# Kernel optimization log

Hardware: AMD Instinct MI355X
Metric: run time of the kernel (lower is better)

The kernel has to match this reference:

```python
import jax, jax.numpy as jnp
import numpy as np

B, N, D, H = 2, 2048, 1024, 16
HD = D // H

def setup_inputs() -> dict:
    key = jax.random.key(0)
    ks = jax.random.split(key, 5)
    s_in = 1.0 / np.sqrt(D)
    x = jax.random.normal(ks[0], (B, N, D), dtype=jnp.float32)
    W_qkv = jax.random.uniform(ks[1], (3 * D, D), minval=-s_in, maxval=s_in, dtype=jnp.float32)
    b_qkv = jax.random.uniform(ks[2], (3 * D,), minval=-s_in, maxval=s_in, dtype=jnp.float32)
    W_out = jax.random.uniform(ks[3], (D, D), minval=-s_in, maxval=s_in, dtype=jnp.float32)
    b_out = jax.random.uniform(ks[4], (D,), minval=-s_in, maxval=s_in, dtype=jnp.float32)
    return {"x": x, "W_qkv": W_qkv, "b_qkv": b_qkv, "W_out": W_out, "b_out": b_out}

def reference(x, W_qkv, b_qkv, W_out, b_out):
    scale = HD ** (-0.5)
    qkv = x @ W_qkv.T + b_qkv                       # [B,N,3D]
    q, k, v = jnp.split(qkv, 3, axis=-1)
    # [B,N,D] -> [B,H,N,HD]
    def heads(t):
        return t.reshape(B, N, H, HD).transpose(0, 2, 1, 3)
    q, k, v = heads(q), heads(k), heads(v)
    attn = jnp.einsum('bhqd,bhkd->bhqk', q, k) * scale   # [B,H,N,N]
    causal = jnp.tril(jnp.ones((N, N), dtype=bool))
    attn = jnp.where(causal, attn, -jnp.inf)
    attn = jax.nn.softmax(attn, axis=-1)
    out = jnp.einsum('bhqk,bhkd->bhqd', attn, v)         # [B,H,N,HD]
    out = out.transpose(0, 2, 1, 3).reshape(B, N, D)
    return out @ W_out.T + b_out
```

## Files before the change

kernel.cpp:

```cpp
#include <hip/hip_runtime.h>
#include <hip/hip_bf16.h>

#define Bdim 2
#define Nseq 2048
#define Dmod 1024
#define Hn   16
#define HDim 64

#define XN  (Bdim * Nseq * Dmod)
#define WQN (3 * Dmod * Dmod)
#define WON (Dmod * Dmod)

typedef __attribute__((ext_vector_type(8))) __bf16 bf16x8;
typedef __attribute__((ext_vector_type(4))) __bf16 bf16x4;
typedef __attribute__((ext_vector_type(4))) float  floatx4;

__device__ __forceinline__ floatx4 mfma16(bf16x8 a, bf16x8 b, floatx4 c) {
    return __builtin_amdgcn_mfma_f32_16x16x32_bf16(a, b, c, 0, 0, 0);
}

__device__ __forceinline__ float exp2v(float x) {
    return __builtin_amdgcn_exp2f(x);
}

__device__ __forceinline__ void async_copy16(__bf16* l, const __bf16* g) {
    __builtin_amdgcn_global_load_lds(
        (const __attribute__((address_space(1))) void*)g,
        (__attribute__((address_space(3))) void*)l,
        16, 0, 0);
}

__global__ __launch_bounds__(256) void convert_kernel(
    const float* __restrict__ x, const float* __restrict__ wq,
    const float* __restrict__ wo,
    __bf16* __restrict__ xb, __bf16* __restrict__ wqb, __bf16* __restrict__ wob)
{
    int i = (blockIdx.x * 256 + threadIdx.x) * 8;
    const float* src;
    __bf16* dst;
    int off;
    if (i < XN)            { src = x;  dst = xb;  off = i; }
    else if (i < XN + WQN) { src = wq; dst = wqb; off = i - XN; }
    else                   { src = wo; dst = wob; off = i - XN - WQN; }
    float4 v0 = *(const float4*)(src + off);
    float4 v1 = *(const float4*)(src + off + 4);
    bf16x8 o;
    o[0] = (__bf16)v0.x; o[1] = (__bf16)v0.y; o[2] = (__bf16)v0.z; o[3] = (__bf16)v0.w;
    o[4] = (__bf16)v1.x; o[5] = (__bf16)v1.y; o[6] = (__bf16)v1.z; o[7] = (__bf16)v1.w;
    *(bf16x8*)(dst + off) = o;
}

__global__ __launch_bounds__(256) void qkv_kernel(
    const __bf16* __restrict__ x, const __bf16* __restrict__ Wq,
    const float* __restrict__ bq,
    __bf16* __restrict__ qb, __bf16* __restrict__ kb, __bf16* __restrict__ vt)
{
    __shared__ __align__(16) __bf16 ldsA[128 * 32];
    __shared__ __align__(16) __bf16 ldsB[128 * 32];

    const int tid  = threadIdx.x;
    const int lane = tid & 63, l16 = lane & 15, quad = lane >> 4;
    const int wiw  = tid >> 6;
    const int wm   = wiw & 1, wn = wiw >> 1;

    const int bm = blockIdx.x & 31;
    const int bn = blockIdx.x >> 5;
    const int m0 = bm * 128, n0 = bn * 128;

    const int srow = tid >> 2;
    const int scol = (tid & 3) * 8;

    floatx4 z = {0.f, 0.f, 0.f, 0.f};
    floatx4 acc[4][4];
    #pragma unroll
    for (int mt = 0; mt < 4; ++mt)
        #pragma unroll
        for (int nt = 0; nt < 4; ++nt) acc[mt][nt] = z;

    const __bf16* ga = x  + (size_t)m0 * Dmod;
    const __bf16* gb = Wq + (size_t)n0 * Dmod;

    for (int k0 = 0; k0 < Dmod; k0 += 32) {
        async_copy16(&ldsA[srow * 32 + scol],        ga + (size_t)srow * Dmod + k0 + scol);
        async_copy16(&ldsA[(64 + srow) * 32 + scol], ga + (size_t)(64 + srow) * Dmod + k0 + scol);
        async_copy16(&ldsB[srow * 32 + scol],        gb + (size_t)srow * Dmod + k0 + scol);
        async_copy16(&ldsB[(64 + srow) * 32 + scol], gb + (size_t)(64 + srow) * Dmod + k0 + scol);
        __syncthreads();

        bf16x8 af[4], bfr[4];
        #pragma unroll
        for (int mt = 0; mt < 4; ++mt)
            af[mt] = *(const bf16x8*)&ldsA[(wm * 64 + mt * 16 + l16) * 32 + quad * 8];
        #pragma unroll
        for (int nt = 0; nt < 4; ++nt)
            bfr[nt] = *(const bf16x8*)&ldsB[(wn * 64 + nt * 16 + l16) * 32 + quad * 8];
        #pragma unroll
        for (int mt = 0; mt < 4; ++mt)
            #pragma unroll
            for (int nt = 0; nt < 4; ++nt)
                acc[mt][nt] = mfma16(af[mt], bfr[nt], acc[mt][nt]);
        __syncthreads();
    }

    const int nb    = n0 + wn * 64;
    const int which = nb >> 10;
    const int h     = (nb & 1023) >> 6;
    const int mw    = m0 + wm * 64;
    const int bi    = mw >> 11;
    const int pos0  = mw & (Nseq - 1);

    const float qscale = 0.18033688f;

    #pragma unroll
    for (int nt = 0; nt < 4; ++nt) {
        float bias = bq[nb + nt * 16 + l16];
        int hd = nt * 16 + l16;
        #pragma unroll
        for (int mt = 0; mt < 4; ++mt)
            #pragma unroll
            for (int i = 0; i < 4; ++i) {
                int pos = pos0 + mt * 16 + quad * 4 + i;
                float r = acc[mt][nt][i] + bias;
                if (which == 0)
                    qb[((bi * Hn + h) * Nseq + pos) * HDim + hd] = (__bf16)(r * qscale);
                else if (which == 1)
                    kb[((bi * Hn + h) * Nseq + pos) * HDim + hd] = (__bf16)r;
                else
                    vt[((bi * Hn + h) * HDim + hd) * Nseq + pos] = (__bf16)r;
            }
    }
}

__global__ __launch_bounds__(256, 4) void attn_kernel(
    const __bf16* __restrict__ qbuf, const __bf16* __restrict__ kbuf,
    const __bf16* __restrict__ vtbuf, __bf16* __restrict__ aout)
{
    __shared__ __align__(16) __bf16 ldsK[64 * 64];
    __shared__ __align__(16) __bf16 ldsV[64 * 64];
    __shared__ __align__(16) __bf16 ldsP[4][16 * 72];

    const int tid  = threadIdx.x;
    const int wiw  = tid >> 6;
    const int lane = tid & 63, l16 = lane & 15, quad = lane >> 4;
    const int b    = blockIdx.x;
    const int bh   = b & 31;
    const int g  = b >> 5;
    const int gk = g & 7, r4 = g >> 3;
    int qblk;
    if      (r4 == 0) qblk = 31 - gk;
    else if (r4 == 1) qblk = gk;
    else if (r4 == 2) qblk = 23 - gk;
    else              qblk = 8 + gk;

    const int q0 = qblk * 64 + wiw * 16;

    const __bf16* qs = qbuf  + bh * Nseq * HDim;
    const __bf16* ks = kbuf  + bh * Nseq * HDim;
    const __bf16* vs = vtbuf + bh * HDim * Nseq;

    const int sr  = tid >> 3;
    const int sb  = tid & 7;
    const int swr = (sb ^ (sr & 7)) * 8;
    const int wk0 = sr * 64 + swr;
    const int wk1 = (sr + 32) * 64 + swr;

    bf16x8 qf0 = *(const bf16x8*)(qs + (q0 + l16) * HDim + quad * 8);
    bf16x8 qf1 = *(const bf16x8*)(qs + (q0 + l16) * HDim + 32 + quad * 8);

    floatx4 z = {0.f, 0.f, 0.f, 0.f};
    floatx4 o[4];
    #pragma unroll
    for (int s = 0; s < 4; ++s) o[s] = z;
    floatx4 lacc = z;
    float m_i = -1e30f;

    bf16x8 ones;
    #pragma unroll
    for (int j = 0; j < 8; ++j) ones[j] = (__bf16)1.0f;

    const int   nkt = qblk + 1;
    __bf16* myp = ldsP[wiw];
    const int swz = l16 & 7;

    float4 rk0 = *(const float4*)(ks + (size_t)sr * HDim + sb * 8);
    float4 rk1 = *(const float4*)(ks + (size_t)(sr + 32) * HDim + sb * 8);
    float4 rv0 = *(const float4*)(vs + (size_t)sr * Nseq + sb * 8);
    float4 rv1 = *(const float4*)(vs + (size_t)(sr + 32) * Nseq + sb * 8);

    for (int kt = 0; kt < nkt; ++kt) {
        float4 nk0 = {}, nk1 = {}, nv0 = {}, nv1 = {};
        if (kt + 1 < nkt) {
            const int k0n = (kt + 1) * 64;
            nk0 = *(const float4*)(ks + (size_t)(k0n + sr) * HDim + sb * 8);
            nk1 = *(const float4*)(ks + (size_t)(k0n + sr + 32) * HDim + sb * 8);
            nv0 = *(const float4*)(vs + (size_t)sr * Nseq + k0n + sb * 8);
            nv1 = *(const float4*)(vs + (size_t)(sr + 32) * Nseq + k0n + sb * 8);
        }

        *(float4*)&ldsK[wk0] = rk0;
        *(float4*)&ldsK[wk1] = rk1;
        *(float4*)&ldsV[wk0] = rv0;
        *(float4*)&ldsV[wk1] = rv1;
        __syncthreads();

        const bool last = (kt == nkt - 1);

        floatx4 st[4];
        __builtin_amdgcn_s_setprio(1);
        #pragma unroll
        for (int t = 0; t < 4; ++t) {
            const __bf16* kr = &ldsK[(t * 16 + l16) * 64];
            bf16x8 kf0 = *(const bf16x8*)(kr + ((quad ^ swz) * 8));
            bf16x8 kf1 = *(const bf16x8*)(kr + (((quad + 4) ^ swz) * 8));
            st[t] = mfma16(kf0, qf0, z);
            st[t] = mfma16(kf1, qf1, st[t]);
        }
        __builtin_amdgcn_s_setprio(0);

        float a[16];
        #pragma unroll
        for (int t = 0; t < 4; ++t)
            #pragma unroll
            for (int i = 0; i < 4; ++i) {
                float v = st[t][i];
                if (last) {
                    int kidx = t * 16 + quad * 4 + i;
                    v = (kidx <= wiw * 16 + l16) ? v : -1e30f;
                }
                a[t * 4 + i] = v;
            }

        float m0 = fmaxf(fmaxf(a[0],  a[1]),  a[2]);
        float m1 = fmaxf(fmaxf(a[3],  a[4]),  a[5]);
        float m2 = fmaxf(fmaxf(a[6],  a[7]),  a[8]);
        float m3 = fmaxf(fmaxf(a[9],  a[10]), a[11]);
        float m4 = fmaxf(fmaxf(a[12], a[13]), a[14]);
        float mx = fmaxf(fmaxf(fmaxf(m0, m1), m2),
                         fmaxf(fmaxf(m3, m4), a[15]));
        mx = fmaxf(mx, __shfl_xor(mx, 16));
        mx = fmaxf(mx, __shfl_xor(mx, 32));

        if (__any(mx > m_i + 8.0f)) {
            float mn    = fmaxf(m_i, mx);
            float alpha = exp2v(m_i - mn);
            #pragma unroll
            for (int s = 0; s < 4; ++s)
                #pragma unroll
                for (int i = 0; i < 4; ++i) o[s][i] *= alpha;
            #pragma unroll
            for (int i = 0; i < 4; ++i) lacc[i] *= alpha;
            m_i = mn;
        }

        float p[16];
        #pragma unroll
        for (int j = 0; j < 16; ++j) p[j] = exp2v(a[j] - m_i);

        #pragma unroll
        for (int t = 0; t < 4; ++t) {
            bf16x4 pk;
            pk.x = (__bf16)p[t * 4 + 0]; pk.y = (__bf16)p[t * 4 + 1];
            pk.z = (__bf16)p[t * 4 + 2]; pk.w = (__bf16)p[t * 4 + 3];
            *(bf16x4*)(myp + l16 * 72 + t * 16 + quad * 4) = pk;
        }
        asm volatile("s_waitcnt lgkmcnt(0)" ::: "memory");
        bf16x8 pf0 = *(const bf16x8*)(myp + l16 * 72 + quad * 8);
        bf16x8 pf1 = *(const bf16x8*)(myp + l16 * 72 + 32 + quad * 8);

        __builtin_amdgcn_s_setprio(1);
        lacc = mfma16(ones, pf0, lacc);
        lacc = mfma16(ones, pf1, lacc);

        #pragma unroll
        for (int s = 0; s < 4; ++s) {
            const __bf16* vr = &ldsV[(s * 16 + l16) * 64];
            bf16x8 vf0 = *(const bf16x8*)(vr + ((quad ^ swz) * 8));
            bf16x8 vf1 = *(const bf16x8*)(vr + (((quad + 4) ^ swz) * 8));
            o[s] = mfma16(vf0, pf0, o[s]);
            o[s] = mfma16(vf1, pf1, o[s]);
        }
        __builtin_amdgcn_s_setprio(0);
        __syncthreads();

        rk0 = nk0; rk1 = nk1; rv0 = nv0; rv1 = nv1;
    }

    const float inv = 1.0f / lacc[0];
    const int bi = bh >> 4, h = bh & 15;
    #pragma unroll
    for (int s = 0; s < 4; ++s) {
        bf16x4 ov;
        ov.x = (__bf16)(o[s][0] * inv); ov.y = (__bf16)(o[s][1] * inv);
        ov.z = (__bf16)(o[s][2] * inv); ov.w = (__bf16)(o[s][3] * inv);
        *(bf16x4*)(aout + ((size_t)(bi * Nseq + q0 + l16)) * Dmod
                   + h * 64 + s * 16 + quad * 4) = ov;
    }
}

__global__ __launch_bounds__(256) void proj_kernel(
    const __bf16* __restrict__ ao, const __bf16* __restrict__ Wo,
    const float* __restrict__ bo, float* __restrict__ out)
{
    __shared__ __align__(16) __bf16 ldsA[64 * 32];
    __shared__ __align__(16) __bf16 ldsB[128 * 32];

    const int tid  = threadIdx.x;
    const int lane = tid & 63, l16 = lane & 15, quad = lane >> 4;
    const int wiw  = tid >> 6;
    const int wm   = wiw & 1, wn = wiw >> 1;

    const int bm = blockIdx.x & 63;
    const int bn = blockIdx.x >> 6;
    const int m0 = bm * 64, n0 = bn * 128;

    const int srow = tid >> 2;
    const int scol = (tid & 3) * 8;

    floatx4 z = {0.f, 0.f, 0.f, 0.f};
    floatx4 acc[2][4];
    #pragma unroll
    for (int mt = 0; mt < 2; ++mt)
        #pragma unroll
        for (int nt = 0; nt < 4; ++nt) acc[mt][nt] = z;

    const __bf16* ga = ao + (size_t)m0 * Dmod;
    const __bf16* gb = Wo + (size_t)n0 * Dmod;

    for (int k0 = 0; k0 < Dmod; k0 += 32) {
        async_copy16(&ldsA[srow * 32 + scol],        ga + (size_t)srow * Dmod + k0 + scol);
        async_copy16(&ldsB[srow * 32 + scol],        gb + (size_t)srow * Dmod + k0 + scol);
        async_copy16(&ldsB[(64 + srow) * 32 + scol], gb + (size_t)(64 + srow) * Dmod + k0 + scol);
        __syncthreads();

        bf16x8 af[2], bfr[4];
        #pragma unroll
        for (int mt = 0; mt < 2; ++mt)
            af[mt] = *(const bf16x8*)&ldsA[(wm * 32 + mt * 16 + l16) * 32 + quad * 8];
        #pragma unroll
        for (int nt = 0; nt < 4; ++nt)
            bfr[nt] = *(const bf16x8*)&ldsB[(wn * 64 + nt * 16 + l16) * 32 + quad * 8];
        #pragma unroll
        for (int mt = 0; mt < 2; ++mt)
            #pragma unroll
            for (int nt = 0; nt < 4; ++nt)
                acc[mt][nt] = mfma16(af[mt], bfr[nt], acc[mt][nt]);
        __syncthreads();
    }

    const int nb = n0 + wn * 64;
    const int mw = m0 + wm * 32;
    #pragma unroll
    for (int nt = 0; nt < 4; ++nt) {
        float bias = bo[nb + nt * 16 + l16];
        #pragma unroll
        for (int mt = 0; mt < 2; ++mt)
            #pragma unroll
            for (int i = 0; i < 4; ++i) {
                int m = mw + mt * 16 + quad * 4 + i;
                out[(size_t)m * Dmod + nb + nt * 16 + l16] = acc[mt][nt][i] + bias;
            }
    }
}

extern "C" void kernel_launch(void* const* d_in, const int* in_sizes, int n_in,
                              void* d_out, int out_size, void* d_ws, size_t ws_size,
                              hipStream_t stream) {
    const float* x  = (const float*)d_in[0];
    const float* Wq = (const float*)d_in[1];
    const float* bq = (const float*)d_in[2];
    const float* Wo = (const float*)d_in[3];
    const float* bo = (const float*)d_in[4];
    float* out = (float*)d_out;

    __bf16* ws  = (__bf16*)d_ws;
    __bf16* xb  = ws;
    __bf16* wqb = ws + (size_t)XN;
    __bf16* wob = wqb + (size_t)WQN;
    __bf16* qb  = wob + (size_t)WON;
    const size_t SZ = (size_t)Bdim * Hn * Nseq * HDim;
    __bf16* kb  = qb + SZ;
    __bf16* vt  = kb + SZ;
    __bf16* ao  = vt + SZ;

    convert_kernel<<<dim3(4096), dim3(256), 0, stream>>>(x, Wq, Wo, xb, wqb, wob);
    qkv_kernel<<<dim3(768), dim3(256), 0, stream>>>(xb, wqb, bq, qb, kb, vt);
    attn_kernel<<<dim3(1024), dim3(256), 0, stream>>>(qb, kb, vt, ao);
    proj_kernel<<<dim3(512), dim3(256), 0, stream>>>(ao, wob, bo, out);
}
```

Before: 174.5 us.

## Double K-tile depth with XOR-swizzled LDS and XCD-aware block mapping in GEMMs

The QKV and output-projection GEMMs now stage 64-wide K slices per iteration instead of 32, which halves the number of barrier pairs per K sweep. Each LDS row gets an XOR swizzle on its 16-byte chunks so the fragment reads avoid bank conflicts. Block indices are also remapped: in the QKV GEMM each XCD is given a contiguous group of N-tiles, and the projection GEMM walks N fastest, both to improve L2 reuse of the weights. LDS use per block doubles, which may lower occupancy.

```diff
diff --git a/kernel.cpp b/kernel.cpp
--- a/kernel.cpp
+++ b/kernel.cpp
@@ -55,20 +55,24 @@
     const float* __restrict__ bq,
     __bf16* __restrict__ qb, __bf16* __restrict__ kb, __bf16* __restrict__ vt)
 {
-    __shared__ __align__(16) __bf16 ldsA[128 * 32];
-    __shared__ __align__(16) __bf16 ldsB[128 * 32];
+    __shared__ __align__(16) __bf16 ldsA[128 * 64];
+    __shared__ __align__(16) __bf16 ldsB[128 * 64];
 
     const int tid  = threadIdx.x;
     const int lane = tid & 63, l16 = lane & 15, quad = lane >> 4;
     const int wiw  = tid >> 6;
     const int wm   = wiw & 1, wn = wiw >> 1;
-
-    const int bm = blockIdx.x & 31;
-    const int bn = blockIdx.x >> 5;
+    const int swq  = l16 & 7;
+
+    const int xcd = blockIdx.x & 7;
+    const int loc = blockIdx.x >> 3;
+    const int bn  = xcd * 3 + loc % 3;
+    const int bm  = loc / 3;
     const int m0 = bm * 128, n0 = bn * 128;
 
-    const int srow = tid >> 2;
-    const int scol = (tid & 3) * 8;
+    const int srow = tid >> 3;
+    const int sdst = srow * 64 + (tid & 7) * 8;
+    const int ssrc = ((tid & 7) ^ (srow & 7)) * 8;
 
     floatx4 z = {0.f, 0.f, 0.f, 0.f};
     floatx4 acc[4][4];
@@ -80,25 +84,33 @@
     const __bf16* ga = x  + (size_t)m0 * Dmod;
     const __bf16* gb = Wq + (size_t)n0 * Dmod;
 
-    for (int k0 = 0; k0 < Dmod; k0 += 32) {
-        async_copy16(&ldsA[srow * 32 + scol],        ga + (size_t)srow * Dmod + k0 + scol);
-        async_copy16(&ldsA[(64 + srow) * 32 + scol], ga + (size_t)(64 + srow) * Dmod + k0 + scol);
-        async_copy16(&ldsB[srow * 32 + scol],        gb + (size_t)srow * Dmod + k0 + scol);
-        async_copy16(&ldsB[(64 + srow) * 32 + scol], gb + (size_t)(64 + srow) * Dmod + k0 + scol);
-        __syncthreads();
-
-        bf16x8 af[4], bfr[4];
-        #pragma unroll
-        for (int mt = 0; mt < 4; ++mt)
-            af[mt] = *(const bf16x8*)&ldsA[(wm * 64 + mt * 16 + l16) * 32 + quad * 8];
-        #pragma unroll
-        for (int nt = 0; nt < 4; ++nt)
-            bfr[nt] = *(const bf16x8*)&ldsB[(wn * 64 + nt * 16 + l16) * 32 + quad * 8];
-        #pragma unroll
-        for (int mt = 0; mt < 4; ++mt)
+    for (int k0 = 0; k0 < Dmod; k0 += 64) {
+        #pragma unroll
+        for (int j = 0; j < 4; ++j) {
+            async_copy16(&ldsA[j * 2048 + sdst],
+                         ga + (size_t)(j * 32 + srow) * Dmod + k0 + ssrc);
+            async_copy16(&ldsB[j * 2048 + sdst],
+                         gb + (size_t)(j * 32 + srow) * Dmod + k0 + ssrc);
+        }
+        __syncthreads();
+
+        #pragma unroll
+        for (int kk = 0; kk < 2; ++kk) {
+            bf16x8 af[4], bfr[4];
+            #pragma unroll
+            for (int mt = 0; mt < 4; ++mt)
+                af[mt] = *(const bf16x8*)&ldsA[(wm * 64 + mt * 16 + l16) * 64
+                                               + (((kk << 2) | quad) ^ swq) * 8];
             #pragma unroll
             for (int nt = 0; nt < 4; ++nt)
-                acc[mt][nt] = mfma16(af[mt], bfr[nt], acc[mt][nt]);
+                bfr[nt] = *(const bf16x8*)&ldsB[(wn * 64 + nt * 16 + l16) * 64
+                                                + (((kk << 2) | quad) ^ swq) * 8];
+            #pragma unroll
+            for (int mt = 0; mt < 4; ++mt)
+                #pragma unroll
+                for (int nt = 0; nt < 4; ++nt)
+                    acc[mt][nt] = mfma16(af[mt], bfr[nt], acc[mt][nt]);
+        }
         __syncthreads();
     }
 
@@ -301,20 +313,22 @@
     const __bf16* __restrict__ ao, const __bf16* __restrict__ Wo,
     const float* __restrict__ bo, float* __restrict__ out)
 {
-    __shared__ __align__(16) __bf16 ldsA[64 * 32];
-    __shared__ __align__(16) __bf16 ldsB[128 * 32];
+    __shared__ __align__(16) __bf16 ldsA[64 * 64];
+    __shared__ __align__(16) __bf16 ldsB[128 * 64];
 
     const int tid  = threadIdx.x;
     const int lane = tid & 63, l16 = lane & 15, quad = lane >> 4;
     const int wiw  = tid >> 6;
     const int wm   = wiw & 1, wn = wiw >> 1;
-
-    const int bm = blockIdx.x & 63;
-    const int bn = blockIdx.x >> 6;
+    const int swq  = l16 & 7;
+
+    const int bn = blockIdx.x & 7;
+    const int bm = blockIdx.x >> 3;
     const int m0 = bm * 64, n0 = bn * 128;
 
-    const int srow = tid >> 2;
-    const int scol = (tid & 3) * 8;
+    const int srow = tid >> 3;
+    const int sdst = srow * 64 + (tid & 7) * 8;
+    const int ssrc = ((tid & 7) ^ (srow & 7)) * 8;
 
     floatx4 z = {0.f, 0.f, 0.f, 0.f};
     floatx4 acc[2][4];
@@ -326,24 +340,34 @@
     const __bf16* ga = ao + (size_t)m0 * Dmod;
     const __bf16* gb = Wo + (size_t)n0 * Dmod;
 
-    for (int k0 = 0; k0 < Dmod; k0 += 32) {
-        async_copy16(&ldsA[srow * 32 + scol],        ga + (size_t)srow * Dmod + k0 + scol);
-        async_copy16(&ldsB[srow * 32 + scol],        gb + (size_t)srow * Dmod + k0 + scol);
-        async_copy16(&ldsB[(64 + srow) * 32 + scol], gb + (size_t)(64 + srow) * Dmod + k0 + scol);
-        __syncthreads();
-
-        bf16x8 af[2], bfr[4];
-        #pragma unroll
-        for (int mt = 0; mt < 2; ++mt)
-            af[mt] = *(const bf16x8*)&ldsA[(wm * 32 + mt * 16 + l16) * 32 + quad * 8];
-        #pragma unroll
-        for (int nt = 0; nt < 4; ++nt)
-            bfr[nt] = *(const bf16x8*)&ldsB[(wn * 64 + nt * 16 + l16) * 32 + quad * 8];
-        #pragma unroll
-        for (int mt = 0; mt < 2; ++mt)
+    for (int k0 = 0; k0 < Dmod; k0 += 64) {
+        #pragma unroll
+        for (int j = 0; j < 2; ++j)
+            async_copy16(&ldsA[j * 2048 + sdst],
+                         ga + (size_t)(j * 32 + srow) * Dmod + k0 + ssrc);
+        #pragma unroll
+        for (int j = 0; j < 4; ++j)
+            async_copy16(&ldsB[j * 2048 + sdst],
+                         gb + (size_t)(j * 32 + srow) * Dmod + k0 + ssrc);
+        __syncthreads();
+
+        #pragma unroll
+        for (int kk = 0; kk < 2; ++kk) {
+            bf16x8 af[2], bfr[4];
+            #pragma unroll
+            for (int mt = 0; mt < 2; ++mt)
+                af[mt] = *(const bf16x8*)&ldsA[(wm * 32 + mt * 16 + l16) * 64
+                                               + (((kk << 2) | quad) ^ swq) * 8];
             #pragma unroll
             for (int nt = 0; nt < 4; ++nt)
-                acc[mt][nt] = mfma16(af[mt], bfr[nt], acc[mt][nt]);
+                bfr[nt] = *(const bf16x8*)&ldsB[(wn * 64 + nt * 16 + l16) * 64
+                                                + (((kk << 2) | quad) ^ swq) * 8];
+            #pragma unroll
+            for (int mt = 0; mt < 2; ++mt)
+                #pragma unroll
+                for (int nt = 0; nt < 4; ++nt)
+                    acc[mt][nt] = mfma16(af[mt], bfr[nt], acc[mt][nt]);
+        }
         __syncthreads();
     }
 
```

Result: slower. 182.5 us (+4.6%).

## Load K and V fragments directly from global memory, dropping LDS staging

Applied to the files above, without the earlier changes.

The attention kernel stops staging K and V tiles through shared memory with register prefetch and block-wide barriers. Each wave now reads its MFMA fragments for K and transposed V straight from global memory, relying on L2/L1 caching to serve the four waves that share a tile. This removes the LDS writes and two __syncthreads per iteration, and frees LDS for occupancy. The cost is four times the global/L1 traffic, less coalesced 16-byte loads, and no explicit prefetch to hide latency.

```diff
diff --git a/kernel.cpp b/kernel.cpp
--- a/kernel.cpp
+++ b/kernel.cpp
@@ -135,8 +135,6 @@
     const __bf16* __restrict__ qbuf, const __bf16* __restrict__ kbuf,
     const __bf16* __restrict__ vtbuf, __bf16* __restrict__ aout)
 {
-    __shared__ __align__(16) __bf16 ldsK[64 * 64];
-    __shared__ __align__(16) __bf16 ldsV[64 * 64];
     __shared__ __align__(16) __bf16 ldsP[4][16 * 72];
 
     const int tid  = threadIdx.x;
@@ -158,12 +156,6 @@
     const __bf16* ks = kbuf  + bh * Nseq * HDim;
     const __bf16* vs = vtbuf + bh * HDim * Nseq;
 
-    const int sr  = tid >> 3;
-    const int sb  = tid & 7;
-    const int swr = (sb ^ (sr & 7)) * 8;
-    const int wk0 = sr * 64 + swr;
-    const int wk1 = (sr + 32) * 64 + swr;
-
     bf16x8 qf0 = *(const bf16x8*)(qs + (q0 + l16) * HDim + quad * 8);
     bf16x8 qf1 = *(const bf16x8*)(qs + (q0 + l16) * HDim + 32 + quad * 8);
 
@@ -180,38 +172,21 @@
 
     const int   nkt = qblk + 1;
     __bf16* myp = ldsP[wiw];
-    const int swz = l16 & 7;
-
-    float4 rk0 = *(const float4*)(ks + (size_t)sr * HDim + sb * 8);
-    float4 rk1 = *(const float4*)(ks + (size_t)(sr + 32) * HDim + sb * 8);
-    float4 rv0 = *(const float4*)(vs + (size_t)sr * Nseq + sb * 8);
-    float4 rv1 = *(const float4*)(vs + (size_t)(sr + 32) * Nseq + sb * 8);
+
+    const __bf16* krow = ks + (size_t)l16 * HDim;
+    const __bf16* vrow = vs + (size_t)l16 * Nseq;
 
     for (int kt = 0; kt < nkt; ++kt) {
-        float4 nk0 = {}, nk1 = {}, nv0 = {}, nv1 = {};
-        if (kt + 1 < nkt) {
-            const int k0n = (kt + 1) * 64;
-            nk0 = *(const float4*)(ks + (size_t)(k0n + sr) * HDim + sb * 8);
-            nk1 = *(const float4*)(ks + (size_t)(k0n + sr + 32) * HDim + sb * 8);
-            nv0 = *(const float4*)(vs + (size_t)sr * Nseq + k0n + sb * 8);
-            nv1 = *(const float4*)(vs + (size_t)(sr + 32) * Nseq + k0n + sb * 8);
-        }
-
-        *(float4*)&ldsK[wk0] = rk0;
-        *(float4*)&ldsK[wk1] = rk1;
-        *(float4*)&ldsV[wk0] = rv0;
-        *(float4*)&ldsV[wk1] = rv1;
-        __syncthreads();
-
+        const int k0 = kt * 64;
         const bool last = (kt == nkt - 1);
 
         floatx4 st[4];
         __builtin_amdgcn_s_setprio(1);
         #pragma unroll
         for (int t = 0; t < 4; ++t) {
-            const __bf16* kr = &ldsK[(t * 16 + l16) * 64];
-            bf16x8 kf0 = *(const bf16x8*)(kr + ((quad ^ swz) * 8));
-            bf16x8 kf1 = *(const bf16x8*)(kr + (((quad + 4) ^ swz) * 8));
+            const __bf16* kr = krow + (size_t)(k0 + t * 16) * HDim;
+            bf16x8 kf0 = *(const bf16x8*)(kr + quad * 8);
+            bf16x8 kf1 = *(const bf16x8*)(kr + 32 + quad * 8);
             st[t] = mfma16(kf0, qf0, z);
             st[t] = mfma16(kf1, qf1, st[t]);
         }
@@ -273,16 +248,13 @@
 
         #pragma unroll
         for (int s = 0; s < 4; ++s) {
-            const __bf16* vr = &ldsV[(s * 16 + l16) * 64];
-            bf16x8 vf0 = *(const bf16x8*)(vr + ((quad ^ swz) * 8));
-            bf16x8 vf1 = *(const bf16x8*)(vr + (((quad + 4) ^ swz) * 8));
+            const __bf16* vr = vrow + (size_t)(s * 16) * Nseq + k0;
+            bf16x8 vf0 = *(const bf16x8*)(vr + quad * 8);
+            bf16x8 vf1 = *(const bf16x8*)(vr + 32 + quad * 8);
             o[s] = mfma16(vf0, pf0, o[s]);
             o[s] = mfma16(vf1, pf1, o[s]);
         }
         __builtin_amdgcn_s_setprio(0);
-        __syncthreads();
-
-        rk0 = nk0; rk1 = nk1; rv0 = nv0; rv1 = nv1;
     }
 
     const float inv = 1.0f / lacc[0];
```

Result: slower. 260.4 us (+49.2%).

## Process two 16-row query tiles per wave in attention to reuse K/V tiles

Applied to the files above, without the earlier changes.

Each attention wave now handles 32 query rows as two 16-row MFMA tiles, so a block covers 128 queries and each K/V tile loaded into LDS serves twice as many rows. The grid is halved to 512 blocks, the causal load-balancing order is simplified to pair blocks 15-gk with gk, and masking now covers the last two key tiles. The aim is to cut global K/V traffic and LDS fragment reads per unit of work. The cost is more registers, so launch bounds drop to 2 blocks per SM, and fewer, larger blocks reduce parallelism and make causal load balance coarser.

```diff
diff --git a/kernel.cpp b/kernel.cpp
--- a/kernel.cpp
+++ b/kernel.cpp
@@ -131,13 +131,13 @@
     }
 }
 
-__global__ __launch_bounds__(256, 4) void attn_kernel(
+__global__ __launch_bounds__(256, 2) void attn_kernel(
     const __bf16* __restrict__ qbuf, const __bf16* __restrict__ kbuf,
     const __bf16* __restrict__ vtbuf, __bf16* __restrict__ aout)
 {
     __shared__ __align__(16) __bf16 ldsK[64 * 64];
     __shared__ __align__(16) __bf16 ldsV[64 * 64];
-    __shared__ __align__(16) __bf16 ldsP[4][16 * 72];
+    __shared__ __align__(16) __bf16 ldsP[4][2 * 16 * 72];
 
     const int tid  = threadIdx.x;
     const int wiw  = tid >> 6;
@@ -145,14 +145,12 @@
     const int b    = blockIdx.x;
     const int bh   = b & 31;
     const int g  = b >> 5;
-    const int gk = g & 7, r4 = g >> 3;
-    int qblk;
-    if      (r4 == 0) qblk = 31 - gk;
-    else if (r4 == 1) qblk = gk;
-    else if (r4 == 2) qblk = 23 - gk;
-    else              qblk = 8 + gk;
-
-    const int q0 = qblk * 64 + wiw * 16;
+    const int gk = g & 7;
+    const int qblk = (g >> 3) == 0 ? 15 - gk : gk;
+
+    const int q0w   = qblk * 128 + wiw * 32;
+    const int qloc0 = wiw * 32 + l16;
+    const int qloc1 = qloc0 + 16;
 
     const __bf16* qs = qbuf  + bh * Nseq * HDim;
     const __bf16* ks = kbuf  + bh * Nseq * HDim;
@@ -164,21 +162,23 @@
     const int wk0 = sr * 64 + swr;
     const int wk1 = (sr + 32) * 64 + swr;
 
-    bf16x8 qf0 = *(const bf16x8*)(qs + (q0 + l16) * HDim + quad * 8);
-    bf16x8 qf1 = *(const bf16x8*)(qs + (q0 + l16) * HDim + 32 + quad * 8);
+    bf16x8 qf00 = *(const bf16x8*)(qs + (q0w + l16) * HDim + quad * 8);
+    bf16x8 qf01 = *(const bf16x8*)(qs + (q0w + l16) * HDim + 32 + quad * 8);
+    bf16x8 qf10 = *(const bf16x8*)(qs + (q0w + 16 + l16) * HDim + quad * 8);
+    bf16x8 qf11 = *(const bf16x8*)(qs + (q0w + 16 + l16) * HDim + 32 + quad * 8);
 
     floatx4 z = {0.f, 0.f, 0.f, 0.f};
-    floatx4 o[4];
-    #pragma unroll
-    for (int s = 0; s < 4; ++s) o[s] = z;
-    floatx4 lacc = z;
-    float m_i = -1e30f;
+    floatx4 o[4][2];
+    #pragma unroll
+    for (int s = 0; s < 4; ++s) { o[s][0] = z; o[s][1] = z; }
+    floatx4 lacc0 = z, lacc1 = z;
+    float m_i0 = -1e30f, m_i1 = -1e30f;
 
     bf16x8 ones;
     #pragma unroll
     for (int j = 0; j < 8; ++j) ones[j] = (__bf16)1.0f;
 
-    const int   nkt = qblk + 1;
+    const int nkt = 2 * qblk + 2;
     __bf16* myp = ldsP[wiw];
     const int swz = l16 & 7;
 
@@ -203,81 +203,107 @@
         *(float4*)&ldsV[wk1] = rv1;
         __syncthreads();
 
-        const bool last = (kt == nkt - 1);
-
-        floatx4 st[4];
+        floatx4 st[4][2];
         __builtin_amdgcn_s_setprio(1);
         #pragma unroll
         for (int t = 0; t < 4; ++t) {
             const __bf16* kr = &ldsK[(t * 16 + l16) * 64];
             bf16x8 kf0 = *(const bf16x8*)(kr + ((quad ^ swz) * 8));
             bf16x8 kf1 = *(const bf16x8*)(kr + (((quad + 4) ^ swz) * 8));
-            st[t] = mfma16(kf0, qf0, z);
-            st[t] = mfma16(kf1, qf1, st[t]);
+            st[t][0] = mfma16(kf0, qf00, z);
+            st[t][0] = mfma16(kf1, qf01, st[t][0]);
+            st[t][1] = mfma16(kf0, qf10, z);
+            st[t][1] = mfma16(kf1, qf11, st[t][1]);
         }
         __builtin_amdgcn_s_setprio(0);
 
-        float a[16];
+        const bool maskt = (kt >= nkt - 2);
+        const int  koff  = kt * 64 - qblk * 128;
+        float a0[16], a1[16];
         #pragma unroll
         for (int t = 0; t < 4; ++t)
             #pragma unroll
             for (int i = 0; i < 4; ++i) {
-                float v = st[t][i];
-                if (last) {
-                    int kidx = t * 16 + quad * 4 + i;
-                    v = (kidx <= wiw * 16 + l16) ? v : -1e30f;
+                float v0 = st[t][0][i], v1 = st[t][1][i];
+                if (maskt) {
+                    int kidx = koff + t * 16 + quad * 4 + i;
+                    v0 = (kidx <= qloc0) ? v0 : -1e30f;
+                    v1 = (kidx <= qloc1) ? v1 : -1e30f;
                 }
-                a[t * 4 + i] = v;
+                a0[t * 4 + i] = v0;
+                a1[t * 4 + i] = v1;
             }
 
-        float m0 = fmaxf(fmaxf(a[0],  a[1]),  a[2]);
-        float m1 = fmaxf(fmaxf(a[3],  a[4]),  a[5]);
-        float m2 = fmaxf(fmaxf(a[6],  a[7]),  a[8]);
-        float m3 = fmaxf(fmaxf(a[9],  a[10]), a[11]);
-        float m4 = fmaxf(fmaxf(a[12], a[13]), a[14]);
-        float mx = fmaxf(fmaxf(fmaxf(m0, m1), m2),
-                         fmaxf(fmaxf(m3, m4), a[15]));
-        mx = fmaxf(mx, __shfl_xor(mx, 16));
-        mx = fmaxf(mx, __shfl_xor(mx, 32));
-
-        if (__any(mx > m_i + 8.0f)) {
-            float mn    = fmaxf(m_i, mx);
-            float alpha = exp2v(m_i - mn);
+        float x0 = fmaxf(fmaxf(a0[0], a0[1]), a0[2]);
+        float x1 = fmaxf(fmaxf(a0[3], a0[4]), a0[5]);
+        float x2 = fmaxf(fmaxf(a0[6], a0[7]), a0[8]);
+        float x3 = fmaxf(fmaxf(a0[9], a0[10]), a0[11]);
+        float x4 = fmaxf(fmaxf(a0[12], a0[13]), a0[14]);
+        float mx0 = fmaxf(fmaxf(fmaxf(x0, x1), x2), fmaxf(fmaxf(x3, x4), a0[15]));
+        mx0 = fmaxf(mx0, __shfl_xor(mx0, 16));
+        mx0 = fmaxf(mx0, __shfl_xor(mx0, 32));
+        float y0 = fmaxf(fmaxf(a1[0], a1[1]), a1[2]);
+        float y1 = fmaxf(fmaxf(a1[3], a1[4]), a1[5]);
+        float y2 = fmaxf(fmaxf(a1[6], a1[7]), a1[8]);
+        float y3 = fmaxf(fmaxf(a1[9], a1[10]), a1[11]);
+        float y4 = fmaxf(fmaxf(a1[12], a1[13]), a1[14]);
+        float mx1 = fmaxf(fmaxf(fmaxf(y0, y1), y2), fmaxf(fmaxf(y3, y4), a1[15]));
+        mx1 = fmaxf(mx1, __shfl_xor(mx1, 16));
+        mx1 = fmaxf(mx1, __shfl_xor(mx1, 32));
+
+        if (__any((mx0 > m_i0 + 8.0f) || (mx1 > m_i1 + 8.0f))) {
+            float mn0 = fmaxf(m_i0, mx0), mn1 = fmaxf(m_i1, mx1);
+            float al0 = exp2v(m_i0 - mn0), al1 = exp2v(m_i1 - mn1);
             #pragma unroll
             for (int s = 0; s < 4; ++s)
                 #pragma unroll
-                for (int i = 0; i < 4; ++i) o[s][i] *= alpha;
-            #pragma unroll
-            for (int i = 0; i < 4; ++i) lacc[i] *= alpha;
-            m_i = mn;
-        }
-
-        float p[16];
-        #pragma unroll
-        for (int j = 0; j < 16; ++j) p[j] = exp2v(a[j] - m_i);
+                for (int i = 0; i < 4; ++i) {
+                    o[s][0][i] *= al0;
+                    o[s][1][i] *= al1;
+                }
+            #pragma unroll
+            for (int i = 0; i < 4; ++i) { lacc0[i] *= al0; lacc1[i] *= al1; }
+            m_i0 = mn0; m_i1 = mn1;
+        }
+
+        float p0[16], p1[16];
+        #pragma unroll
+        for (int j = 0; j < 16; ++j) {
+            p0[j] = exp2v(a0[j] - m_i0);
+            p1[j] = exp2v(a1[j] - m_i1);
+        }
 
         #pragma unroll
         for (int t = 0; t < 4; ++t) {
-            bf16x4 pk;
-            pk.x = (__bf16)p[t * 4 + 0]; pk.y = (__bf16)p[t * 4 + 1];
-            pk.z = (__bf16)p[t * 4 + 2]; pk.w = (__bf16)p[t * 4 + 3];
-            *(bf16x4*)(myp + l16 * 72 + t * 16 + quad * 4) = pk;
+            bf16x4 pk0, pk1;
+            pk0.x = (__bf16)p0[t * 4 + 0]; pk0.y = (__bf16)p0[t * 4 + 1];
+            pk0.z = (__bf16)p0[t * 4 + 2]; pk0.w = (__bf16)p0[t * 4 + 3];
+            pk1.x = (__bf16)p1[t * 4 + 0]; pk1.y = (__bf16)p1[t * 4 + 1];
+            pk1.z = (__bf16)p1[t * 4 + 2]; pk1.w = (__bf16)p1[t * 4 + 3];
+            *(bf16x4*)(myp + l16 * 72 + t * 16 + quad * 4)        = pk0;
+            *(bf16x4*)(myp + 1152 + l16 * 72 + t * 16 + quad * 4) = pk1;
         }
         asm volatile("s_waitcnt lgkmcnt(0)" ::: "memory");
-        bf16x8 pf0 = *(const bf16x8*)(myp + l16 * 72 + quad * 8);
-        bf16x8 pf1 = *(const bf16x8*)(myp + l16 * 72 + 32 + quad * 8);
+        bf16x8 pf00 = *(const bf16x8*)(myp + l16 * 72 + quad * 8);
+        bf16x8 pf01 = *(const bf16x8*)(myp + l16 * 72 + 32 + quad * 8);
+        bf16x8 pf10 = *(const bf16x8*)(myp + 1152 + l16 * 72 + quad * 8);
+        bf16x8 pf11 = *(const bf16x8*)(myp + 1152 + l16 * 72 + 32 + quad * 8);
 
         __builtin_amdgcn_s_setprio(1);
-        lacc = mfma16(ones, pf0, lacc);
-        lacc = mfma16(ones, pf1, lacc);
+        lacc0 = mfma16(ones, pf00, lacc0);
+        lacc0 = mfma16(ones, pf01, lacc0);
+        lacc1 = mfma16(ones, pf10, lacc1);
+        lacc1 = mfma16(ones, pf11, lacc1);
 
         #pragma unroll
         for (int s = 0; s < 4; ++s) {
             const __bf16* vr = &ldsV[(s * 16 + l16) * 64];
             bf16x8 vf0 = *(const bf16x8*)(vr + ((quad ^ swz) * 8));
             bf16x8 vf1 = *(const bf16x8*)(vr + (((quad + 4) ^ swz) * 8));
-            o[s] = mfma16(vf0, pf0, o[s]);
-            o[s] = mfma16(vf1, pf1, o[s]);
+            o[s][0] = mfma16(vf0, pf00, o[s][0]);
+            o[s][0] = mfma16(vf1, pf01, o[s][0]);
+            o[s][1] = mfma16(vf0, pf10, o[s][1]);
+            o[s][1] = mfma16(vf1, pf11, o[s][1]);
         }
         __builtin_amdgcn_s_setprio(0);
         __syncthreads();
@@ -285,15 +311,20 @@
         rk0 = nk0; rk1 = nk1; rv0 = nv0; rv1 = nv1;
     }
 
-    const float inv = 1.0f / lacc[0];
+    const float inv0 = 1.0f / lacc0[0];
+    const float inv1 = 1.0f / lacc1[0];
     const int bi = bh >> 4, h = bh & 15;
     #pragma unroll
     for (int s = 0; s < 4; ++s) {
-        bf16x4 ov;
-        ov.x = (__bf16)(o[s][0] * inv); ov.y = (__bf16)(o[s][1] * inv);
-        ov.z = (__bf16)(o[s][2] * inv); ov.w = (__bf16)(o[s][3] * inv);
-        *(bf16x4*)(aout + ((size_t)(bi * Nseq + q0 + l16)) * Dmod
-                   + h * 64 + s * 16 + quad * 4) = ov;
+        bf16x4 ov0, ov1;
+        ov0.x = (__bf16)(o[s][0][0] * inv0); ov0.y = (__bf16)(o[s][0][1] * inv0);
+        ov0.z = (__bf16)(o[s][0][2] * inv0); ov0.w = (__bf16)(o[s][0][3] * inv0);
+        ov1.x = (__bf16)(o[s][1][0] * inv1); ov1.y = (__bf16)(o[s][1][1] * inv1);
+        ov1.z = (__bf16)(o[s][1][2] * inv1); ov1.w = (__bf16)(o[s][1][3] * inv1);
+        *(bf16x4*)(aout + ((size_t)(bi * Nseq + q0w + l16)) * Dmod
+                   + h * 64 + s * 16 + quad * 4) = ov0;
+        *(bf16x4*)(aout + ((size_t)(bi * Nseq + q0w + 16 + l16)) * Dmod
+                   + h * 64 + s * 16 + quad * 4) = ov1;
     }
 }
 
@@ -384,6 +415,6 @@
 
     convert_kernel<<<dim3(4096), dim3(256), 0, stream>>>(x, Wq, Wo, xb, wqb, wob);
     qkv_kernel<<<dim3(768), dim3(256), 0, stream>>>(xb, wqb, bq, qb, kb, vt);
-    attn_kernel<<<dim3(1024), dim3(256), 0, stream>>>(qb, kb, vt, ao);
+    attn_kernel<<<dim3(512), dim3(256), 0, stream>>>(qb, kb, vt, ao);
     proj_kernel<<<dim3(512), dim3(256), 0, stream>>>(ao, wob, bo, out);
 }
```

New measurement: 182.7 us. 1.05x slower.
